# Optimization experiments

Measured on AMD Instinct MI355X. Metric: run time of the kernel, lower is better.

## Reference

```python
import jax, jax.numpy as jnp
import numpy as np

EPS = 1e-5  # torch BatchNorm default eps


def _bn(x, gamma, beta, axes):
    # training-mode batch norm over `axes`, channel dim is axis 1
    mean = jnp.mean(x, axis=axes, keepdims=True)
    var = jnp.var(x, axis=axes, keepdims=True)
    shape = [1] * x.ndim
    shape[1] = -1
    return (x - mean) * jax.lax.rsqrt(var + EPS) * gamma.reshape(shape) + beta.reshape(shape)


def setup_inputs() -> dict:
    B, C, N = 16, 512, 192
    S_RATIO, R_RATIO = 4, 8
    Cs, Cr = C // S_RATIO, C // R_RATIO  # 128, 64
    inter = N * Cr + C  # 12800
    key = jax.random.key(0)
    ks = jax.random.split(key, 6)

    def w(k, shp, fan):
        return jax.random.normal(k, shp, jnp.float32) * np.float32(np.sqrt(2.0 / fan))

    return {
        "inputs": jax.random.normal(ks[0], (B, C, N), jnp.float32),
        "retain": 0,
        "theta_w": w(ks[1], (Cs, C), Cs), "theta_b": jnp.zeros((Cs,), jnp.float32),
        "theta_g": jnp.ones((Cs,), jnp.float32), "theta_be": jnp.zeros((Cs,), jnp.float32),
        "phi_w": w(ks[2], (Cs, C), Cs), "phi_b": jnp.zeros((Cs,), jnp.float32),
        "phi_g": jnp.ones((Cs,), jnp.float32), "phi_be": jnp.zeros((Cs,), jnp.float32),
        "re_w": w(ks[3], (Cr, Cs), Cr), "re_b": jnp.zeros((Cr,), jnp.float32),
        "re_g": jnp.ones((Cr,), jnp.float32), "re_be": jnp.zeros((Cr,), jnp.float32),
        "att_w": w(ks[4], (C, inter), C), "att_b": jnp.zeros((C,), jnp.float32),
        "att_g": jnp.ones((C,), jnp.float32), "att_be": jnp.zeros((C,), jnp.float32),
    }


def reference(inputs, retain, theta_w, theta_b, theta_g, theta_be,
              phi_w, phi_b, phi_g, phi_be, re_w, re_b, re_g, re_be,
              att_w, att_b, att_g, att_be):
    B, C, N = inputs.shape
    xt = inputs.transpose(0, 2, 1)  # [B, N, C]

    # theta / phi pro_blocks: Linear -> BN1d (over B,N) -> ReLU, output [B, Cs, N]
    th = jax.nn.relu(_bn(jnp.einsum('bnc,oc->bon', xt, theta_w) + theta_b[None, :, None], theta_g, theta_be, (0, 2)))
    ph = jax.nn.relu(_bn(jnp.einsum('bnc,oc->bon', xt, phi_w) + phi_b[None, :, None], phi_g, phi_be, (0, 2)))
    th = th.transpose(0, 2, 1)  # [B, N, Cs]
    ph = ph.transpose(0, 2, 1)  # [B, N, Cs]

    # pairwise broadcast-diff: [B, N, N, Cs]
    diff = th[:, :, None, :] - ph[:, None, :, :]

    # pro_block1: Linear -> BN2d -> ReLU, then flatten to [B, N, N*Cr]
    rel = jnp.einsum('bijc,oc->boij', diff, re_w) + re_b[None, :, None, None]  # [B, Cr, N, N]
    rel = jax.nn.relu(_bn(rel, re_g, re_be, (0, 2, 3)))
    rel = rel.transpose(0, 2, 3, 1).reshape(B, N, -1)  # [B, N, N*Cr]

    # attention_generator: Linear -> BN1d -> sigmoid, output [B, C, N]
    cat = jnp.concatenate([xt, rel], axis=2)  # [B, N, C + N*Cr]
    att = jnp.einsum('bni,oi->bon', cat, att_w) + att_b[None, :, None]  # [B, C, N]
    att = jax.nn.sigmoid(_bn(att, att_g, att_be, (0, 2)))

    features = att * inputs  # [B, C, N]
    if retain:
        return features
    return jnp.sum(features, axis=2) / jnp.sum(att, axis=2)  # [B, C]
```

## Files before the change

kernel.cpp:

```cpp
#include <hip/hip_runtime.h>

#define BB 16
#define CC 512
#define NN 192
#define CS 128
#define CR 64
#define EPSF 1e-5f
#define PART (BB*CC*NN)

typedef __attribute__((ext_vector_type(8))) short short8;
typedef __attribute__((ext_vector_type(4))) float f32x4;
typedef __attribute__((ext_vector_type(4))) unsigned int uint4v;

#define OFF_LIN2  0
#define OFF_ATTPX 0
#define OFF_A     1572864
#define OFF_B     1769472
#define OFF_P2    1966080
#define OFF_QT    2162688
#define OFF_ATTP3 2359296
#define OFF_WBF   7077888
#define OFF_XT    10354688
#define OFF_ROWS  11141120
#define OFF_SCL   11157504

__device__ __forceinline__ unsigned pkbf(float a, float b){
  unsigned r; asm("v_cvt_pk_bf16_f32 %0, %1, %2" : "=v"(r) : "v"(a), "v"(b)); return r;
}

__device__ __forceinline__ void gload_lds16(const void* g, void* l){
  __builtin_amdgcn_global_load_lds(
      (const __attribute__((address_space(1))) unsigned int*)g,
      (__attribute__((address_space(3))) unsigned int*)l, 16, 0, 0);
}

__global__ __launch_bounds__(256) void kconvxt(
    const float* __restrict__ aw, const float* __restrict__ x,
    short* __restrict__ wbf, short* __restrict__ xT)
{
  __shared__ float Ts[64][65];
  if (blockIdx.x < 3200) {
    int t = blockIdx.x*256 + threadIdx.x;
    int o2 = t / 1600;
    int kk = (t - o2*1600) * 8;
    const float* src = &aw[o2*12800 + kk];
    float4 v0 = *reinterpret_cast<const float4*>(src);
    float4 v1 = *reinterpret_cast<const float4*>(src+4);
    uint4v w;
    w.x = pkbf(v0.x, v0.y); w.y = pkbf(v0.z, v0.w);
    w.z = pkbf(v1.x, v1.y); w.w = pkbf(v1.z, v1.w);
    *reinterpret_cast<uint4v*>(&wbf[o2*12800 + kk]) = w;
  } else {
    int bid = blockIdx.x - 3200;
    int nt = bid % 3; int ct = (bid/3) & 7; int b = bid / 24;
    int c0 = ct*64, n0 = nt*64;
    int tid = threadIdx.x;
    int col = tid & 63, r0 = tid >> 6;
    #pragma unroll
    for (int it = 0; it < 16; ++it){
      int r = r0 + it*4;
      Ts[r][col] = x[(b*CC + c0 + r)*NN + n0 + col];
    }
    __syncthreads();
    #pragma unroll
    for (int it = 0; it < 2; ++it){
      int cp = it*256 + tid;
      int nr = cp >> 3, cc8 = (cp & 7)*8;
      uint4v wv;
      wv.x = pkbf(Ts[cc8+0][nr], Ts[cc8+1][nr]);
      wv.y = pkbf(Ts[cc8+2][nr], Ts[cc8+3][nr]);
      wv.z = pkbf(Ts[cc8+4][nr], Ts[cc8+5][nr]);
      wv.w = pkbf(Ts[cc8+6][nr], Ts[cc8+7][nr]);
      *reinterpret_cast<uint4v*>(&xT[((b*NN) + n0 + nr)*CC + c0 + cc8]) = wv;
    }
  }
}

__global__ __launch_bounds__(256) void k1_lin(
    const float* __restrict__ x, const float* __restrict__ wth,
    const float* __restrict__ wph, float* __restrict__ lin2)
{
  int bid = blockIdx.x;
  int nt = bid % 3; int ch = (bid/3) & 1; int b = (bid/6) & 15; int path = bid/96;
  int cs0 = ch*64, n0 = nt*64;
  const float* w = path ? wph : wth;
  int tid = threadIdx.x;
  int ty = tid >> 4, tx = tid & 15;
  __shared__ float Xs[32][64];
  __shared__ float Ws[32][68];
  float acc[4][4];
  #pragma unroll
  for (int i=0;i<4;++i)
    #pragma unroll
    for (int j=0;j<4;++j) acc[i][j]=0.f;
  for (int c0 = 0; c0 < CC; c0 += 32){
    __syncthreads();
    {
      int nn = tid & 63, cb = tid >> 6;
      #pragma unroll
      for (int it = 0; it < 8; ++it)
        Xs[cb + it*4][nn] = x[(b*CC + c0 + cb + it*4)*NN + n0 + nn];
    }
    {
      int cc = tid & 31, sb = tid >> 5;
      #pragma unroll
      for (int it = 0; it < 8; ++it)
        Ws[cc][sb + it*8] = w[(cs0 + sb + it*8)*CC + c0 + cc];
    }
    __syncthreads();
    #pragma unroll 8
    for (int cc = 0; cc < 32; ++cc){
      float w4[4], x4[4];
      *reinterpret_cast<float4*>(w4) = *reinterpret_cast<const float4*>(&Ws[cc][ty*4]);
      *reinterpret_cast<float4*>(x4) = *reinterpret_cast<const float4*>(&Xs[cc][tx*4]);
      #pragma unroll
      for (int i=0;i<4;++i)
        #pragma unroll
        for (int j=0;j<4;++j) acc[i][j] += w4[i]*x4[j];
    }
  }
  #pragma unroll
  for (int r = 0; r < 4; ++r){
    int cs = cs0 + ty*4 + r;
    float4 v = make_float4(acc[r][0],acc[r][1],acc[r][2],acc[r][3]);
    *reinterpret_cast<float4*>(&lin2[(b*256 + path*128 + cs)*NN + n0 + tx*4]) = v;
  }
}

__global__ __launch_bounds__(256) void k2_stats(
    const float* __restrict__ lin2,
    const float* __restrict__ tg, const float* __restrict__ tbe,
    const float* __restrict__ pg, const float* __restrict__ pbe,
    float* __restrict__ scl)
{
  int cs2 = blockIdx.x;
  const float* src = lin2 + cs2*NN;
  int tid = threadIdx.x;
  float s=0.f, q=0.f;
  for (int e = tid; e < BB*NN; e += 256){
    int b = e / NN, n = e - b*NN;
    float v = src[b*256*NN + n];
    s += v; q += v*v;
  }
  __shared__ float rs[4], rq[4];
  #pragma unroll
  for (int off=32; off; off>>=1){ s += __shfl_down(s,off); q += __shfl_down(q,off); }
  int w = tid >> 6;
  if ((tid & 63)==0){ rs[w]=s; rq[w]=q; }
  __syncthreads();
  if (tid==0){
    s = rs[0]+rs[1]+rs[2]+rs[3]; q = rq[0]+rq[1]+rq[2]+rq[3];
    float mean = s * (1.f/3072.f);
    float var = q * (1.f/3072.f) - mean*mean;
    int path = cs2 >> 7, c = cs2 & 127;
    float g  = path ? pg[c]  : tg[c];
    float be = path ? pbe[c] : tbe[c];
    float a = g * rsqrtf(var + EPSF);
    scl[cs2] = a; scl[256+cs2] = be - mean*a;
  }
}

__global__ __launch_bounds__(256) void k3_gemm(
    const float* __restrict__ lin2, const float* __restrict__ scl,
    const float* __restrict__ rw,
    float* __restrict__ A, float* __restrict__ Bq, float* __restrict__ rows4)
{
  int bid = blockIdx.x;
  int ih = bid & 3; int b = (bid>>2) & 15; int path = bid >> 6;
  int i0 = ih*48;
  __shared__ float Ls[128][48];
  __shared__ float Ws[64][132];
  int tid = threadIdx.x;
  #pragma unroll
  for (int it = 0; it < 6; ++it){
    int cp = it*256 + tid;
    int row = cp / 12, c4 = cp - row*12;
    float a = scl[path*128 + row], d = scl[256 + path*128 + row];
    float4 v = *reinterpret_cast<const float4*>(&lin2[(b*256 + path*128 + row)*NN + i0 + c4*4]);
    float4 r;
    r.x = fmaxf(a*v.x + d, 0.f); r.y = fmaxf(a*v.y + d, 0.f);
    r.z = fmaxf(a*v.z + d, 0.f); r.w = fmaxf(a*v.w + d, 0.f);
    *reinterpret_cast<float4*>(&Ls[row][c4*4]) = r;
  }
  #pragma unroll
  for (int it = 0; it < 8; ++it){
    int cp = it*256 + tid;
    int o = cp >> 5, c4 = cp & 31;
    *reinterpret_cast<float4*>(&Ws[o][c4*4]) =
      *reinterpret_cast<const float4*>(&rw[o*CS + c4*4]);
  }
  __syncthreads();
  int oy = tid >> 4, ix = tid & 15;
  float acc[4][3];
  #pragma unroll
  for (int r=0;r<4;++r)
    #pragma unroll
    for (int e=0;e<3;++e) acc[r][e]=0.f;
  #pragma unroll 4
  for (int c = 0; c < 128; ++c){
    float w4[4], l3[3];
    #pragma unroll
    for (int r=0;r<4;++r) w4[r] = Ws[oy*4+r][c];
    #pragma unroll
    for (int e=0;e<3;++e) l3[e] = Ls[c][ix*3+e];
    #pragma unroll
    for (int r=0;r<4;++r)
      #pragma unroll
      for (int e=0;e<3;++e) acc[r][e] += w4[r]*l3[e];
  }
  float* dst = path ? Bq : A;
  #pragma unroll
  for (int r=0;r<4;++r)
    #pragma unroll
    for (int e=0;e<3;++e)
      dst[(b*CR + oy*4+r)*NN + i0 + ix*3 + e] = acc[r][e];
  #pragma unroll
  for (int r=0;r<4;++r){
    float s = acc[r][0]+acc[r][1]+acc[r][2];
    float q = acc[r][0]*acc[r][0]+acc[r][1]*acc[r][1]+acc[r][2]*acc[r][2];
    #pragma unroll
    for (int off=8; off; off>>=1){ s += __shfl_down(s,off,16); q += __shfl_down(q,off,16); }
    if (ix==0){
      int o = oy*4+r;
      int ri = (path*1024 + b*64 + o)*4 + ih;
      rows4[ri] = s; rows4[8192 + ri] = q;
    }
  }
}

__global__ void k4_relstats(const float* __restrict__ rows4,
    const float* __restrict__ rg, const float* __restrict__ rbe,
    float* __restrict__ scl)
{
  int o = threadIdx.x;
  float sa=0,saq=0,sb=0,sbq=0,cross=0;
  for (int b=0;b<BB;++b){
    float ra=0, rb=0;
    #pragma unroll
    for (int ih=0; ih<4; ++ih){
      int ia = (b*64+o)*4 + ih, ib = (1024 + b*64+o)*4 + ih;
      ra += rows4[ia]; rb += rows4[ib];
      saq += rows4[8192 + ia]; sbq += rows4[8192 + ib];
    }
    sa += ra; sb += rb; cross += ra*rb;
  }
  float mean = (sa - sb) * (1.f/3072.f);
  float e2 = (saq + sbq) * (1.f/3072.f) - cross * (2.f/589824.f);
  float var = e2 - mean*mean;
  float s = rg[o] * rsqrtf(var + EPSF);
  scl[512+o] = s;
  scl[576+o] = rbe[o] - s*mean;
}

__global__ __launch_bounds__(256) void k4_pq(
    const float* __restrict__ A, const float* __restrict__ Bq,
    const float* __restrict__ scl, float* __restrict__ p2,
    float* __restrict__ qT)
{
  int idx = blockIdx.x*256 + threadIdx.x;
  const int TOT = BB*CR*NN;
  int path = idx / TOT; int e = idx - path*TOT;
  int b = e / (CR*NN); int rem = e - b*(CR*NN);
  if (path == 0) {
    int n = rem >> 6, o = rem & 63;
    p2[e] = scl[512+o]*A[b*CR*NN + o*NN + n] + scl[576+o];
  } else {
    int j = rem >> 6, o = rem & 63;
    qT[e] = scl[512+o]*Bq[b*CR*NN + o*NN + j];
  }
}

__global__ __launch_bounds__(256) void k5_mfma(
    const short* __restrict__ wbf, const short* __restrict__ xT,
    const float* __restrict__ p2, const float* __restrict__ qT,
    float* __restrict__ attpx, float* __restrict__ attp3)
{
  int bid = blockIdx.x;
  int nt = bid & 1, mt = (bid >> 1) & 3, b = (bid >> 3) & 15, ks = bid >> 7;
  int o20 = mt*128, n0 = nt*96;
  int j0 = ks*48;

  int tid = threadIdx.x;
  int w = tid >> 6, lane = tid & 63;
  int wr = w >> 1, wc = w & 1;
  int l15 = lane & 15, l4 = lane >> 4;
  int cq = tid & 7;

  __shared__ __align__(16) short As[128*64];
  __shared__ __align__(16) short Bs[96*64];
  __shared__ __align__(16) float qlds[2][64];

  float pr[3][8];
  #pragma unroll
  for (int it=0; it<3; ++it){
    int n = it*32 + (tid >> 3);
    const float* pp = &p2[((b*NN) + n0 + n)*64 + cq*8];
    float4 u0 = *reinterpret_cast<const float4*>(pp);
    float4 u1 = *reinterpret_cast<const float4*>(pp+4);
    pr[it][0]=u0.x; pr[it][1]=u0.y; pr[it][2]=u0.z; pr[it][3]=u0.w;
    pr[it][4]=u1.x; pr[it][5]=u1.y; pr[it][6]=u1.z; pr[it][7]=u1.w;
  }
  if (tid < 64) qlds[0][tid] = qT[(b*NN + j0)*64 + tid];

  auto stageA = [&](int colbase){
    #pragma unroll
    for (int it=0; it<4; ++it){
      int cp = w*256 + it*64 + lane;
      int row = cp >> 3, c = (cp & 7) ^ (row & 7);
      gload_lds16(&wbf[(o20 + row)*12800 + colbase + c*8],
                  &As[(w*256 + it*64)*8]);
    }
  };
  auto stageBx = [&](int colbase){
    #pragma unroll
    for (int it=0; it<3; ++it){
      int cp = w*192 + it*64 + lane;
      int row = cp >> 3, c = (cp & 7) ^ (row & 7);
      gload_lds16(&xT[((b*NN) + n0 + row)*CC + colbase + c*8],
                  &Bs[(w*192 + it*64)*8]);
    }
  };

  f32x4 acc[4][3];
  #pragma unroll
  for (int mi=0;mi<4;++mi)
    #pragma unroll
    for (int ni=0;ni<3;++ni) acc[mi][ni] = (f32x4){0.f,0.f,0.f,0.f};

  auto mfma_phase = [&](){
    #pragma unroll
    for (int s=0; s<2; ++s){
      short8 av[4], bv[3];
      int c = s*4 + l4;
      #pragma unroll
      for (int mi=0; mi<4; ++mi){
        int row = wr*64 + mi*16 + l15;
        av[mi] = *reinterpret_cast<const short8*>(&As[row*64 + ((c ^ (row&7))<<3)]);
      }
      #pragma unroll
      for (int ni=0; ni<3; ++ni){
        int rown = wc*48 + ni*16 + l15;
        bv[ni] = *reinterpret_cast<const short8*>(&Bs[rown*64 + ((c ^ (rown&7))<<3)]);
      }
      #pragma unroll
      for (int mi=0; mi<4; ++mi)
        #pragma unroll
        for (int ni=0; ni<3; ++ni)
          acc[mi][ni] = __builtin_amdgcn_mfma_f32_16x16x32_bf16(av[mi], bv[ni], acc[mi][ni], 0, 0, 0);
    }
  };

  for (int kt = 0; kt < 2; ++kt){
    __syncthreads();
    stageA(ks*128 + kt*64);
    stageBx(ks*128 + kt*64);
    __syncthreads();
    mfma_phase();
  }
  for (int kt = 0; kt < 48; ++kt){
    int j = j0 + kt;
    __syncthreads();
    stageA(512 + j*64);
    if (tid < 64 && kt < 47) qlds[(kt+1)&1][tid] = qT[(b*NN + j + 1)*64 + tid];
    {
      const float* qq = qlds[kt&1];
      float4 qa = *reinterpret_cast<const float4*>(&qq[cq*8]);
      float4 qb = *reinterpret_cast<const float4*>(&qq[cq*8+4]);
      #pragma unroll
      for (int it=0; it<3; ++it){
        float r0 = fmaxf(pr[it][0]-qa.x, 0.f);
        float r1 = fmaxf(pr[it][1]-qa.y, 0.f);
        float r2 = fmaxf(pr[it][2]-qa.z, 0.f);
        float r3 = fmaxf(pr[it][3]-qa.w, 0.f);
        float r4 = fmaxf(pr[it][4]-qb.x, 0.f);
        float r5 = fmaxf(pr[it][5]-qb.y, 0.f);
        float r6 = fmaxf(pr[it][6]-qb.z, 0.f);
        float r7 = fmaxf(pr[it][7]-qb.w, 0.f);
        uint4v wv;
        wv.x = pkbf(r0,r1); wv.y = pkbf(r2,r3);
        wv.z = pkbf(r4,r5); wv.w = pkbf(r6,r7);
        int n = it*32 + (tid >> 3);
        *reinterpret_cast<uint4v*>(&Bs[n*64 + ((cq ^ (n&7))<<3)]) = wv;
      }
    }
    __syncthreads();
    mfma_phase();
  }

  float* dst = (ks == 0) ? attpx : (attp3 + (size_t)(ks-1)*PART);
  #pragma unroll
  for (int mi=0; mi<4; ++mi){
    #pragma unroll
    for (int r=0; r<4; ++r){
      int o2 = o20 + wr*64 + mi*16 + l4*4 + r;
      #pragma unroll
      for (int ni=0; ni<3; ++ni){
        int n = n0 + wc*48 + ni*16 + l15;
        dst[(b*CC + o2)*NN + n] = acc[mi][ni][r];
      }
    }
  }
}

__global__ __launch_bounds__(256) void k67(
    const float* __restrict__ px, const float* __restrict__ p3,
    const float* __restrict__ x,
    const float* __restrict__ g, const float* __restrict__ be,
    float* __restrict__ out)
{
  int o2 = blockIdx.x;
  int tid = threadIdx.x;
  int b = tid >> 4, nl = tid & 15;
  int base = (b*CC + o2)*NN + nl;
  float v[12], xv[12];
  float s=0.f, q=0.f;
  #pragma unroll
  for (int it=0; it<12; ++it){
    int idx = base + it*16;
    float t = px[idx] + p3[idx] + p3[PART+idx] + p3[2*PART+idx];
    v[it] = t; s += t; q += t*t;
    xv[it] = x[idx];
  }
  __shared__ float rs[4], rq[4], ad[2];
  #pragma unroll
  for (int off=32; off; off>>=1){ s += __shfl_down(s,off); q += __shfl_down(q,off); }
  int w = tid >> 6;
  if ((tid & 63)==0){ rs[w]=s; rq[w]=q; }
  __syncthreads();
  if (tid==0){
    s = rs[0]+rs[1]+rs[2]+rs[3]; q = rq[0]+rq[1]+rq[2]+rq[3];
    float mean = s * (1.f/3072.f);
    float var = q * (1.f/3072.f) - mean*mean;
    float a = g[o2] * rsqrtf(var + EPSF);
    ad[0] = a; ad[1] = be[o2] - mean*a;
  }
  __syncthreads();
  float a = ad[0], d = ad[1];
  float sf=0.f, ss=0.f;
  #pragma unroll
  for (int it=0; it<12; ++it){
    float sig = 1.f/(1.f + expf(-(a*v[it] + d)));
    sf += sig * xv[it]; ss += sig;
  }
  #pragma unroll
  for (int off=8; off; off>>=1){ sf += __shfl_down(sf,off,16); ss += __shfl_down(ss,off,16); }
  if (nl==0) out[b*CC + o2] = sf/ss;
}

extern "C" void kernel_launch(void* const* d_in, const int* in_sizes, int n_in,
                              void* d_out, int out_size, void* d_ws, size_t ws_size,
                              hipStream_t stream)
{
  const float* inputs  = (const float*)d_in[0];
  const float* theta_w = (const float*)d_in[2];
  const float* theta_g = (const float*)d_in[4];
  const float* theta_be= (const float*)d_in[5];
  const float* phi_w   = (const float*)d_in[6];
  const float* phi_g   = (const float*)d_in[8];
  const float* phi_be  = (const float*)d_in[9];
  const float* re_w    = (const float*)d_in[10];
  const float* re_g    = (const float*)d_in[12];
  const float* re_be   = (const float*)d_in[13];
  const float* att_w   = (const float*)d_in[14];
  const float* att_g   = (const float*)d_in[16];
  const float* att_be  = (const float*)d_in[17];

  float* ws = (float*)d_ws;
  float* lin2  = ws + OFF_LIN2;
  float* attpx = ws + OFF_ATTPX;
  float* Abuf  = ws + OFF_A;
  float* Bbuf  = ws + OFF_B;
  float* p2buf = ws + OFF_P2;
  float* qTbuf = ws + OFF_QT;
  float* attp3 = ws + OFF_ATTP3;
  short* wbf   = (short*)(ws + OFF_WBF);
  short* xT    = (short*)(ws + OFF_XT);
  float* rows4 = ws + OFF_ROWS;
  float* scl   = ws + OFF_SCL;

  kconvxt<<<3584, 256, 0, stream>>>(att_w, inputs, wbf, xT);
  k1_lin<<<192, 256, 0, stream>>>(inputs, theta_w, phi_w, lin2);
  k2_stats<<<256, 256, 0, stream>>>(lin2, theta_g, theta_be, phi_g, phi_be, scl);
  k3_gemm<<<128, 256, 0, stream>>>(lin2, scl, re_w, Abuf, Bbuf, rows4);
  k4_relstats<<<1, 64, 0, stream>>>(rows4, re_g, re_be, scl);
  k4_pq<<<1536, 256, 0, stream>>>(Abuf, Bbuf, scl, p2buf, qTbuf);
  k5_mfma<<<512, 256, 0, stream>>>(wbf, xT, p2buf, qTbuf, attpx, attp3);
  k67<<<512, 256, 0, stream>>>(attpx, attp3, inputs, att_g, att_be, (float*)d_out);
}
```

Baseline: 136.0 us.

## Fuse BN stats into linear kernel, drop pq kernel, build B operands in registers

Computes per-channel partial sums inside k1_lin and replaces the stats kernel with a single-block finalize. k3_gemm now writes raw p/q in transposed layout, and the BN scale/shift is applied inside k5_mfma, which removes the separate k4_pq kernel. k5_mfma also builds its B operand fragments directly in registers instead of staging them through LDS, which drops the Bs buffer and its stores and reads. The aim is fewer launches, less global traffic and less LDS traffic. The cost is more register pressure in k5, now with a launch-bounds hint, and uncoalesced short8 global loads of xT.

```diff
diff --git a/kernel.cpp b/kernel.cpp
--- a/kernel.cpp
+++ b/kernel.cpp
@@ -14,15 +14,14 @@
 
 #define OFF_LIN2  0
 #define OFF_ATTPX 0
-#define OFF_A     1572864
-#define OFF_B     1769472
-#define OFF_P2    1966080
-#define OFF_QT    2162688
-#define OFF_ATTP3 2359296
-#define OFF_WBF   7077888
-#define OFF_XT    10354688
-#define OFF_ROWS  11141120
-#define OFF_SCL   11157504
+#define OFF_P2    1572864
+#define OFF_QT    1769472
+#define OFF_ATTP3 1966080
+#define OFF_WBF   6684672
+#define OFF_XT    9961472
+#define OFF_ROWS  10747904
+#define OFF_SPART 10764288
+#define OFF_SCL   10788864
 
 __device__ __forceinline__ unsigned pkbf(float a, float b){
   unsigned r; asm("v_cvt_pk_bf16_f32 %0, %1, %2" : "=v"(r) : "v"(a), "v"(b)); return r;
@@ -78,7 +77,8 @@
 
 __global__ __launch_bounds__(256) void k1_lin(
     const float* __restrict__ x, const float* __restrict__ wth,
-    const float* __restrict__ wph, float* __restrict__ lin2)
+    const float* __restrict__ wph, float* __restrict__ lin2,
+    float* __restrict__ spart)
 {
   int bid = blockIdx.x;
   int nt = bid % 3; int ch = (bid/3) & 1; int b = (bid/6) & 15; int path = bid/96;
@@ -125,45 +125,44 @@
     float4 v = make_float4(acc[r][0],acc[r][1],acc[r][2],acc[r][3]);
     *reinterpret_cast<float4*>(&lin2[(b*256 + path*128 + cs)*NN + n0 + tx*4]) = v;
   }
-}
-
-__global__ __launch_bounds__(256) void k2_stats(
-    const float* __restrict__ lin2,
+  #pragma unroll
+  for (int r = 0; r < 4; ++r){
+    float s = acc[r][0]+acc[r][1]+acc[r][2]+acc[r][3];
+    float q = acc[r][0]*acc[r][0]+acc[r][1]*acc[r][1]
+            + acc[r][2]*acc[r][2]+acc[r][3]*acc[r][3];
+    #pragma unroll
+    for (int off=8; off; off>>=1){ s += __shfl_down(s,off,16); q += __shfl_down(q,off,16); }
+    if (tx==0){
+      int cs2 = path*128 + cs0 + ty*4 + r;
+      spart[cs2*48 + b*3 + nt] = s;
+      spart[12288 + cs2*48 + b*3 + nt] = q;
+    }
+  }
+}
+
+__global__ void k2_fin(const float* __restrict__ spart,
     const float* __restrict__ tg, const float* __restrict__ tbe,
     const float* __restrict__ pg, const float* __restrict__ pbe,
     float* __restrict__ scl)
 {
-  int cs2 = blockIdx.x;
-  const float* src = lin2 + cs2*NN;
-  int tid = threadIdx.x;
+  int c2 = threadIdx.x;
   float s=0.f, q=0.f;
-  for (int e = tid; e < BB*NN; e += 256){
-    int b = e / NN, n = e - b*NN;
-    float v = src[b*256*NN + n];
-    s += v; q += v*v;
-  }
-  __shared__ float rs[4], rq[4];
-  #pragma unroll
-  for (int off=32; off; off>>=1){ s += __shfl_down(s,off); q += __shfl_down(q,off); }
-  int w = tid >> 6;
-  if ((tid & 63)==0){ rs[w]=s; rq[w]=q; }
-  __syncthreads();
-  if (tid==0){
-    s = rs[0]+rs[1]+rs[2]+rs[3]; q = rq[0]+rq[1]+rq[2]+rq[3];
-    float mean = s * (1.f/3072.f);
-    float var = q * (1.f/3072.f) - mean*mean;
-    int path = cs2 >> 7, c = cs2 & 127;
-    float g  = path ? pg[c]  : tg[c];
-    float be = path ? pbe[c] : tbe[c];
-    float a = g * rsqrtf(var + EPSF);
-    scl[cs2] = a; scl[256+cs2] = be - mean*a;
-  }
+  #pragma unroll 8
+  for (int i=0;i<48;++i){ s += spart[c2*48+i]; q += spart[12288+c2*48+i]; }
+  float mean = s * (1.f/3072.f);
+  float var = q * (1.f/3072.f) - mean*mean;
+  int path = c2 >> 7, c = c2 & 127;
+  float g  = path ? pg[c]  : tg[c];
+  float be = path ? pbe[c] : tbe[c];
+  float a = g * rsqrtf(var + EPSF);
+  scl[c2] = a; scl[256+c2] = be - mean*a;
 }
 
 __global__ __launch_bounds__(256) void k3_gemm(
     const float* __restrict__ lin2, const float* __restrict__ scl,
     const float* __restrict__ rw,
-    float* __restrict__ A, float* __restrict__ Bq, float* __restrict__ rows4)
+    float* __restrict__ p2raw, float* __restrict__ qTraw,
+    float* __restrict__ rows4)
 {
   int bid = blockIdx.x;
   int ih = bid & 3; int b = (bid>>2) & 15; int path = bid >> 6;
@@ -208,12 +207,12 @@
       #pragma unroll
       for (int e=0;e<3;++e) acc[r][e] += w4[r]*l3[e];
   }
-  float* dst = path ? Bq : A;
+  float* dst = path ? qTraw : p2raw;
   #pragma unroll
   for (int r=0;r<4;++r)
     #pragma unroll
     for (int e=0;e<3;++e)
-      dst[(b*CR + oy*4+r)*NN + i0 + ix*3 + e] = acc[r][e];
+      dst[(b*NN + i0 + ix*3 + e)*64 + oy*4 + r] = acc[r][e];
   #pragma unroll
   for (int r=0;r<4;++r){
     float s = acc[r][0]+acc[r][1]+acc[r][2];
@@ -252,27 +251,10 @@
   scl[576+o] = rbe[o] - s*mean;
 }
 
-__global__ __launch_bounds__(256) void k4_pq(
-    const float* __restrict__ A, const float* __restrict__ Bq,
-    const float* __restrict__ scl, float* __restrict__ p2,
-    float* __restrict__ qT)
-{
-  int idx = blockIdx.x*256 + threadIdx.x;
-  const int TOT = BB*CR*NN;
-  int path = idx / TOT; int e = idx - path*TOT;
-  int b = e / (CR*NN); int rem = e - b*(CR*NN);
-  if (path == 0) {
-    int n = rem >> 6, o = rem & 63;
-    p2[e] = scl[512+o]*A[b*CR*NN + o*NN + n] + scl[576+o];
-  } else {
-    int j = rem >> 6, o = rem & 63;
-    qT[e] = scl[512+o]*Bq[b*CR*NN + o*NN + j];
-  }
-}
-
-__global__ __launch_bounds__(256) void k5_mfma(
+__global__ __launch_bounds__(256, 2) void k5_mfma(
     const short* __restrict__ wbf, const short* __restrict__ xT,
-    const float* __restrict__ p2, const float* __restrict__ qT,
+    const float* __restrict__ p2raw, const float* __restrict__ qTraw,
+    const float* __restrict__ scl,
     float* __restrict__ attpx, float* __restrict__ attp3)
 {
   int bid = blockIdx.x;
@@ -284,23 +266,36 @@
   int w = tid >> 6, lane = tid & 63;
   int wr = w >> 1, wc = w & 1;
   int l15 = lane & 15, l4 = lane >> 4;
-  int cq = tid & 7;
+  int ob = l4*8;
 
   __shared__ __align__(16) short As[128*64];
-  __shared__ __align__(16) short Bs[96*64];
   __shared__ __align__(16) float qlds[2][64];
 
-  float pr[3][8];
-  #pragma unroll
-  for (int it=0; it<3; ++it){
-    int n = it*32 + (tid >> 3);
-    const float* pp = &p2[((b*NN) + n0 + n)*64 + cq*8];
-    float4 u0 = *reinterpret_cast<const float4*>(pp);
-    float4 u1 = *reinterpret_cast<const float4*>(pp+4);
-    pr[it][0]=u0.x; pr[it][1]=u0.y; pr[it][2]=u0.z; pr[it][3]=u0.w;
-    pr[it][4]=u1.x; pr[it][5]=u1.y; pr[it][6]=u1.z; pr[it][7]=u1.w;
-  }
-  if (tid < 64) qlds[0][tid] = qT[(b*NN + j0)*64 + tid];
+  float sq_ = scl[512 + (tid & 63)];
+
+  float pa[3][16];
+  {
+    float sc[16], sh[16];
+    *reinterpret_cast<float4*>(&sc[0])  = *reinterpret_cast<const float4*>(&scl[512+ob]);
+    *reinterpret_cast<float4*>(&sc[4])  = *reinterpret_cast<const float4*>(&scl[512+ob+4]);
+    *reinterpret_cast<float4*>(&sc[8])  = *reinterpret_cast<const float4*>(&scl[512+32+ob]);
+    *reinterpret_cast<float4*>(&sc[12]) = *reinterpret_cast<const float4*>(&scl[512+32+ob+4]);
+    *reinterpret_cast<float4*>(&sh[0])  = *reinterpret_cast<const float4*>(&scl[576+ob]);
+    *reinterpret_cast<float4*>(&sh[4])  = *reinterpret_cast<const float4*>(&scl[576+ob+4]);
+    *reinterpret_cast<float4*>(&sh[8])  = *reinterpret_cast<const float4*>(&scl[576+32+ob]);
+    *reinterpret_cast<float4*>(&sh[12]) = *reinterpret_cast<const float4*>(&scl[576+32+ob+4]);
+    #pragma unroll
+    for (int ni=0; ni<3; ++ni){
+      const float* pb = &p2raw[(size_t)((b*NN) + n0 + wc*48 + ni*16 + l15)*64];
+      float r[16];
+      *reinterpret_cast<float4*>(&r[0])  = *reinterpret_cast<const float4*>(&pb[ob]);
+      *reinterpret_cast<float4*>(&r[4])  = *reinterpret_cast<const float4*>(&pb[ob+4]);
+      *reinterpret_cast<float4*>(&r[8])  = *reinterpret_cast<const float4*>(&pb[32+ob]);
+      *reinterpret_cast<float4*>(&r[12]) = *reinterpret_cast<const float4*>(&pb[32+ob+4]);
+      #pragma unroll
+      for (int k=0;k<16;++k) pa[ni][k] = sc[k]*r[k] + sh[k];
+    }
+  }
 
   auto stageA = [&](int colbase){
     #pragma unroll
@@ -311,15 +306,6 @@
                   &As[(w*256 + it*64)*8]);
     }
   };
-  auto stageBx = [&](int colbase){
-    #pragma unroll
-    for (int it=0; it<3; ++it){
-      int cp = w*192 + it*64 + lane;
-      int row = cp >> 3, c = (cp & 7) ^ (row & 7);
-      gload_lds16(&xT[((b*NN) + n0 + row)*CC + colbase + c*8],
-                  &Bs[(w*192 + it*64)*8]);
-    }
-  };
 
   f32x4 acc[4][3];
   #pragma unroll
@@ -327,10 +313,10 @@
     #pragma unroll
     for (int ni=0;ni<3;++ni) acc[mi][ni] = (f32x4){0.f,0.f,0.f,0.f};
 
-  auto mfma_phase = [&](){
+  auto mfma_phase = [&](short8 bvv[3][2]){
     #pragma unroll
     for (int s=0; s<2; ++s){
-      short8 av[4], bv[3];
+      short8 av[4];
       int c = s*4 + l4;
       #pragma unroll
       for (int mi=0; mi<4; ++mi){
@@ -338,53 +324,61 @@
         av[mi] = *reinterpret_cast<const short8*>(&As[row*64 + ((c ^ (row&7))<<3)]);
       }
       #pragma unroll
-      for (int ni=0; ni<3; ++ni){
-        int rown = wc*48 + ni*16 + l15;
-        bv[ni] = *reinterpret_cast<const short8*>(&Bs[rown*64 + ((c ^ (rown&7))<<3)]);
-      }
-      #pragma unroll
       for (int mi=0; mi<4; ++mi)
         #pragma unroll
         for (int ni=0; ni<3; ++ni)
-          acc[mi][ni] = __builtin_amdgcn_mfma_f32_16x16x32_bf16(av[mi], bv[ni], acc[mi][ni], 0, 0, 0);
+          acc[mi][ni] = __builtin_amdgcn_mfma_f32_16x16x32_bf16(av[mi], bvv[ni][s], acc[mi][ni], 0, 0, 0);
     }
   };
 
-  for (int kt = 0; kt < 2; ++kt){
+  stageA(ks*128);
+  if (tid < 64) qlds[0][tid] = sq_ * qTraw[(size_t)(b*NN + j0)*64 + tid];
+  short8 bvx[3][2];
+  #pragma unroll
+  for (int ni=0; ni<3; ++ni)
+    #pragma unroll
+    for (int s=0; s<2; ++s)
+      bvx[ni][s] = *reinterpret_cast<const short8*>(
+        &xT[(size_t)((b*NN) + n0 + wc*48 + ni*16 + l15)*CC + ks*128 + s*32 + ob]);
+  __syncthreads();
+  mfma_phase(bvx);
+  __syncthreads();
+  stageA(ks*128 + 64);
+  #pragma unroll
+  for (int ni=0; ni<3; ++ni)
+    #pragma unroll
+    for (int s=0; s<2; ++s)
+      bvx[ni][s] = *reinterpret_cast<const short8*>(
+        &xT[(size_t)((b*NN) + n0 + wc*48 + ni*16 + l15)*CC + ks*128 + 64 + s*32 + ob]);
+  __syncthreads();
+  mfma_phase(bvx);
+
+  for (int kt = 0; kt < 48; ++kt){
     __syncthreads();
-    stageA(ks*128 + kt*64);
-    stageBx(ks*128 + kt*64);
+    stageA(512 + (j0 + kt)*64);
+    if (tid < 64 && kt < 47)
+      qlds[(kt+1)&1][tid] = sq_ * qTraw[(size_t)(b*NN + j0 + kt + 1)*64 + tid];
+    const float* qq = qlds[kt&1];
+    float ql[16];
+    *reinterpret_cast<float4*>(&ql[0])  = *reinterpret_cast<const float4*>(&qq[ob]);
+    *reinterpret_cast<float4*>(&ql[4])  = *reinterpret_cast<const float4*>(&qq[ob+4]);
+    *reinterpret_cast<float4*>(&ql[8])  = *reinterpret_cast<const float4*>(&qq[32+ob]);
+    *reinterpret_cast<float4*>(&ql[12]) = *reinterpret_cast<const float4*>(&qq[32+ob+4]);
+    short8 bvv[3][2];
+    #pragma unroll
+    for (int ni=0; ni<3; ++ni){
+      #pragma unroll
+      for (int s=0; s<2; ++s){
+        uint4v u;
+        u.x = pkbf(fmaxf(pa[ni][s*8+0]-ql[s*8+0],0.f), fmaxf(pa[ni][s*8+1]-ql[s*8+1],0.f));
+        u.y = pkbf(fmaxf(pa[ni][s*8+2]-ql[s*8+2],0.f), fmaxf(pa[ni][s*8+3]-ql[s*8+3],0.f));
+        u.z = pkbf(fmaxf(pa[ni][s*8+4]-ql[s*8+4],0.f), fmaxf(pa[ni][s*8+5]-ql[s*8+5],0.f));
+        u.w = pkbf(fmaxf(pa[ni][s*8+6]-ql[s*8+6],0.f), fmaxf(pa[ni][s*8+7]-ql[s*8+7],0.f));
+        bvv[ni][s] = *reinterpret_cast<short8*>(&u);
+      }
+    }
     __syncthreads();
-    mfma_phase();
-  }
-  for (int kt = 0; kt < 48; ++kt){
-    int j = j0 + kt;
-    __syncthreads();
-    stageA(512 + j*64);
-    if (tid < 64 && kt < 47) qlds[(kt+1)&1][tid] = qT[(b*NN + j + 1)*64 + tid];
-    {
-      const float* qq = qlds[kt&1];
-      float4 qa = *reinterpret_cast<const float4*>(&qq[cq*8]);
-      float4 qb = *reinterpret_cast<const float4*>(&qq[cq*8+4]);
-      #pragma unroll
-      for (int it=0; it<3; ++it){
-        float r0 = fmaxf(pr[it][0]-qa.x, 0.f);
-        float r1 = fmaxf(pr[it][1]-qa.y, 0.f);
-        float r2 = fmaxf(pr[it][2]-qa.z, 0.f);
-        float r3 = fmaxf(pr[it][3]-qa.w, 0.f);
-        float r4 = fmaxf(pr[it][4]-qb.x, 0.f);
-        float r5 = fmaxf(pr[it][5]-qb.y, 0.f);
-        float r6 = fmaxf(pr[it][6]-qb.z, 0.f);
-        float r7 = fmaxf(pr[it][7]-qb.w, 0.f);
-        uint4v wv;
-        wv.x = pkbf(r0,r1); wv.y = pkbf(r2,r3);
-        wv.z = pkbf(r4,r5); wv.w = pkbf(r6,r7);
-        int n = it*32 + (tid >> 3);
-        *reinterpret_cast<uint4v*>(&Bs[n*64 + ((cq ^ (n&7))<<3)]) = wv;
-      }
-    }
-    __syncthreads();
-    mfma_phase();
+    mfma_phase(bvv);
   }
 
   float* dst = (ks == 0) ? attpx : (attp3 + (size_t)(ks-1)*PART);
@@ -468,22 +462,20 @@
   float* ws = (float*)d_ws;
   float* lin2  = ws + OFF_LIN2;
   float* attpx = ws + OFF_ATTPX;
-  float* Abuf  = ws + OFF_A;
-  float* Bbuf  = ws + OFF_B;
-  float* p2buf = ws + OFF_P2;
-  float* qTbuf = ws + OFF_QT;
+  float* p2raw = ws + OFF_P2;
+  float* qTraw = ws + OFF_QT;
   float* attp3 = ws + OFF_ATTP3;
   short* wbf   = (short*)(ws + OFF_WBF);
   short* xT    = (short*)(ws + OFF_XT);
   float* rows4 = ws + OFF_ROWS;
+  float* spart = ws + OFF_SPART;
   float* scl   = ws + OFF_SCL;
 
+  k1_lin<<<192, 256, 0, stream>>>(inputs, theta_w, phi_w, lin2, spart);
   kconvxt<<<3584, 256, 0, stream>>>(att_w, inputs, wbf, xT);
-  k1_lin<<<192, 256, 0, stream>>>(inputs, theta_w, phi_w, lin2);
-  k2_stats<<<256, 256, 0, stream>>>(lin2, theta_g, theta_be, phi_g, phi_be, scl);
-  k3_gemm<<<128, 256, 0, stream>>>(lin2, scl, re_w, Abuf, Bbuf, rows4);
+  k2_fin<<<1, 256, 0, stream>>>(spart, theta_g, theta_be, phi_g, phi_be, scl);
+  k3_gemm<<<128, 256, 0, stream>>>(lin2, scl, re_w, p2raw, qTraw, rows4);
   k4_relstats<<<1, 64, 0, stream>>>(rows4, re_g, re_be, scl);
-  k4_pq<<<1536, 256, 0, stream>>>(Abuf, Bbuf, scl, p2buf, qTbuf);
-  k5_mfma<<<512, 256, 0, stream>>>(wbf, xT, p2buf, qTbuf, attpx, attp3);
+  k5_mfma<<<512, 256, 0, stream>>>(wbf, xT, p2raw, qTraw, scl, attpx, attp3);
   k67<<<512, 256, 0, stream>>>(attpx, attp3, inputs, att_g, att_be, (float*)d_out);
 }
```

Result: slower. 140.6 us (+3.4%).

## Fuse prep/linear/stats kernels, fold BN scaling into GEMM, split K wider with atomics

Applied to the files above, without the earlier changes.

Merges the weight/transpose conversion and theta/phi linear into one launch. That launch emits per-tile partial BN statistics, which the relation GEMM reduces itself, removing the separate stats kernel. The relation BN stats and p/q scaling kernels are folded into the main MFMA kernel, which now uses 8 K-splits and 1024 blocks. Results accumulate via atomicAdd into four zeroed partial buffers, which requires a memset of those buffers. The change cuts launch count and intermediate traffic, at the cost of redundant per-block stat reductions, atomic contention and the extra memset.

```diff
diff --git a/kernel.cpp b/kernel.cpp
--- a/kernel.cpp
+++ b/kernel.cpp
@@ -13,16 +13,13 @@
 typedef __attribute__((ext_vector_type(4))) unsigned int uint4v;
 
 #define OFF_LIN2  0
-#define OFF_ATTPX 0
-#define OFF_A     1572864
-#define OFF_B     1769472
-#define OFF_P2    1966080
-#define OFF_QT    2162688
-#define OFF_ATTP3 2359296
-#define OFF_WBF   7077888
-#define OFF_XT    10354688
-#define OFF_ROWS  11141120
-#define OFF_SCL   11157504
+#define OFF_P2    786432
+#define OFF_QT    983040
+#define OFF_ATTP4 1179648
+#define OFF_WBF   7471104
+#define OFF_XT    10747904
+#define OFF_ROWS  11534336
+#define OFF_SPART 11550720
 
 __device__ __forceinline__ unsigned pkbf(float a, float b){
   unsigned r; asm("v_cvt_pk_bf16_f32 %0, %1, %2" : "=v"(r) : "v"(a), "v"(b)); return r;
@@ -34,13 +31,16 @@
       (__attribute__((address_space(3))) unsigned int*)l, 16, 0, 0);
 }
 
-__global__ __launch_bounds__(256) void kconvxt(
+__global__ __launch_bounds__(256) void kprep(
     const float* __restrict__ aw, const float* __restrict__ x,
-    short* __restrict__ wbf, short* __restrict__ xT)
+    const float* __restrict__ wth, const float* __restrict__ wph,
+    short* __restrict__ wbf, short* __restrict__ xT,
+    float* __restrict__ lin2, float* __restrict__ spart)
 {
-  __shared__ float Ts[64][65];
+  __shared__ __align__(16) float smem[4224];
+  int tid = threadIdx.x;
   if (blockIdx.x < 3200) {
-    int t = blockIdx.x*256 + threadIdx.x;
+    int t = blockIdx.x*256 + tid;
     int o2 = t / 1600;
     int kk = (t - o2*1600) * 8;
     const float* src = &aw[o2*12800 + kk];
@@ -50,11 +50,11 @@
     w.x = pkbf(v0.x, v0.y); w.y = pkbf(v0.z, v0.w);
     w.z = pkbf(v1.x, v1.y); w.w = pkbf(v1.z, v1.w);
     *reinterpret_cast<uint4v*>(&wbf[o2*12800 + kk]) = w;
-  } else {
+  } else if (blockIdx.x < 3584) {
+    float (*Ts)[65] = reinterpret_cast<float(*)[65]>(smem);
     int bid = blockIdx.x - 3200;
     int nt = bid % 3; int ct = (bid/3) & 7; int b = bid / 24;
     int c0 = ct*64, n0 = nt*64;
-    int tid = threadIdx.x;
     int col = tid & 63, r0 = tid >> 6;
     #pragma unroll
     for (int it = 0; it < 16; ++it){
@@ -73,109 +73,101 @@
       wv.w = pkbf(Ts[cc8+6][nr], Ts[cc8+7][nr]);
       *reinterpret_cast<uint4v*>(&xT[((b*NN) + n0 + nr)*CC + c0 + cc8]) = wv;
     }
-  }
-}
-
-__global__ __launch_bounds__(256) void k1_lin(
-    const float* __restrict__ x, const float* __restrict__ wth,
-    const float* __restrict__ wph, float* __restrict__ lin2)
-{
-  int bid = blockIdx.x;
-  int nt = bid % 3; int ch = (bid/3) & 1; int b = (bid/6) & 15; int path = bid/96;
-  int cs0 = ch*64, n0 = nt*64;
-  const float* w = path ? wph : wth;
-  int tid = threadIdx.x;
-  int ty = tid >> 4, tx = tid & 15;
-  __shared__ float Xs[32][64];
-  __shared__ float Ws[32][68];
-  float acc[4][4];
-  #pragma unroll
-  for (int i=0;i<4;++i)
-    #pragma unroll
-    for (int j=0;j<4;++j) acc[i][j]=0.f;
-  for (int c0 = 0; c0 < CC; c0 += 32){
-    __syncthreads();
-    {
-      int nn = tid & 63, cb = tid >> 6;
-      #pragma unroll
-      for (int it = 0; it < 8; ++it)
-        Xs[cb + it*4][nn] = x[(b*CC + c0 + cb + it*4)*NN + n0 + nn];
-    }
-    {
-      int cc = tid & 31, sb = tid >> 5;
-      #pragma unroll
-      for (int it = 0; it < 8; ++it)
-        Ws[cc][sb + it*8] = w[(cs0 + sb + it*8)*CC + c0 + cc];
-    }
-    __syncthreads();
-    #pragma unroll 8
-    for (int cc = 0; cc < 32; ++cc){
-      float w4[4], x4[4];
-      *reinterpret_cast<float4*>(w4) = *reinterpret_cast<const float4*>(&Ws[cc][ty*4]);
-      *reinterpret_cast<float4*>(x4) = *reinterpret_cast<const float4*>(&Xs[cc][tx*4]);
-      #pragma unroll
-      for (int i=0;i<4;++i)
+  } else {
+    float (*Xs)[64] = reinterpret_cast<float(*)[64]>(smem);
+    float (*Ws)[68] = reinterpret_cast<float(*)[68]>(smem + 2048);
+    int bid = blockIdx.x - 3584;
+    int nt = bid % 3; int ch = (bid/3) & 1; int b = (bid/6) & 15; int path = bid/96;
+    int cs0 = ch*64, n0 = nt*64;
+    const float* w = path ? wph : wth;
+    int ty = tid >> 4, tx = tid & 15;
+    float acc[4][4];
+    #pragma unroll
+    for (int i=0;i<4;++i)
+      #pragma unroll
+      for (int j=0;j<4;++j) acc[i][j]=0.f;
+    for (int c0 = 0; c0 < CC; c0 += 32){
+      __syncthreads();
+      {
+        int nn = tid & 63, cb = tid >> 6;
         #pragma unroll
-        for (int j=0;j<4;++j) acc[i][j] += w4[i]*x4[j];
-    }
-  }
-  #pragma unroll
-  for (int r = 0; r < 4; ++r){
-    int cs = cs0 + ty*4 + r;
-    float4 v = make_float4(acc[r][0],acc[r][1],acc[r][2],acc[r][3]);
-    *reinterpret_cast<float4*>(&lin2[(b*256 + path*128 + cs)*NN + n0 + tx*4]) = v;
-  }
-}
-
-__global__ __launch_bounds__(256) void k2_stats(
-    const float* __restrict__ lin2,
+        for (int it = 0; it < 8; ++it)
+          Xs[cb + it*4][nn] = x[(b*CC + c0 + cb + it*4)*NN + n0 + nn];
+      }
+      {
+        int cc = tid & 31, sb = tid >> 5;
+        #pragma unroll
+        for (int it = 0; it < 8; ++it)
+          Ws[cc][sb + it*8] = w[(cs0 + sb + it*8)*CC + c0 + cc];
+      }
+      __syncthreads();
+      #pragma unroll 8
+      for (int cc = 0; cc < 32; ++cc){
+        float w4[4], x4[4];
+        *reinterpret_cast<float4*>(w4) = *reinterpret_cast<const float4*>(&Ws[cc][ty*4]);
+        *reinterpret_cast<float4*>(x4) = *reinterpret_cast<const float4*>(&Xs[cc][tx*4]);
+        #pragma unroll
+        for (int i=0;i<4;++i)
+          #pragma unroll
+          for (int j=0;j<4;++j) acc[i][j] += w4[i]*x4[j];
+      }
+    }
+    #pragma unroll
+    for (int r = 0; r < 4; ++r){
+      int cs = cs0 + ty*4 + r;
+      float4 v = make_float4(acc[r][0],acc[r][1],acc[r][2],acc[r][3]);
+      *reinterpret_cast<float4*>(&lin2[(b*256 + path*128 + cs)*NN + n0 + tx*4]) = v;
+    }
+    #pragma unroll
+    for (int r = 0; r < 4; ++r){
+      float s = acc[r][0]+acc[r][1]+acc[r][2]+acc[r][3];
+      float q = acc[r][0]*acc[r][0]+acc[r][1]*acc[r][1]
+              + acc[r][2]*acc[r][2]+acc[r][3]*acc[r][3];
+      #pragma unroll
+      for (int off=8; off; off>>=1){ s += __shfl_down(s,off,16); q += __shfl_down(q,off,16); }
+      if (tx==0){
+        int cs2 = path*128 + cs0 + ty*4 + r;
+        spart[cs2*48 + b*3 + nt] = s;
+        spart[12288 + cs2*48 + b*3 + nt] = q;
+      }
+    }
+  }
+}
+
+__global__ __launch_bounds__(256) void k3_gemm(
+    const float* __restrict__ lin2, const float* __restrict__ spart,
     const float* __restrict__ tg, const float* __restrict__ tbe,
     const float* __restrict__ pg, const float* __restrict__ pbe,
-    float* __restrict__ scl)
-{
-  int cs2 = blockIdx.x;
-  const float* src = lin2 + cs2*NN;
-  int tid = threadIdx.x;
-  float s=0.f, q=0.f;
-  for (int e = tid; e < BB*NN; e += 256){
-    int b = e / NN, n = e - b*NN;
-    float v = src[b*256*NN + n];
-    s += v; q += v*v;
-  }
-  __shared__ float rs[4], rq[4];
-  #pragma unroll
-  for (int off=32; off; off>>=1){ s += __shfl_down(s,off); q += __shfl_down(q,off); }
-  int w = tid >> 6;
-  if ((tid & 63)==0){ rs[w]=s; rq[w]=q; }
-  __syncthreads();
-  if (tid==0){
-    s = rs[0]+rs[1]+rs[2]+rs[3]; q = rq[0]+rq[1]+rq[2]+rq[3];
-    float mean = s * (1.f/3072.f);
-    float var = q * (1.f/3072.f) - mean*mean;
-    int path = cs2 >> 7, c = cs2 & 127;
-    float g  = path ? pg[c]  : tg[c];
-    float be = path ? pbe[c] : tbe[c];
-    float a = g * rsqrtf(var + EPSF);
-    scl[cs2] = a; scl[256+cs2] = be - mean*a;
-  }
-}
-
-__global__ __launch_bounds__(256) void k3_gemm(
-    const float* __restrict__ lin2, const float* __restrict__ scl,
     const float* __restrict__ rw,
-    float* __restrict__ A, float* __restrict__ Bq, float* __restrict__ rows4)
+    float* __restrict__ p2raw, float* __restrict__ qTraw,
+    float* __restrict__ rows4)
 {
   int bid = blockIdx.x;
   int ih = bid & 3; int b = (bid>>2) & 15; int path = bid >> 6;
   int i0 = ih*48;
   __shared__ float Ls[128][48];
   __shared__ float Ws[64][132];
+  __shared__ float sscl[512];
   int tid = threadIdx.x;
+  {
+    int c2 = tid;
+    float s=0.f, q=0.f;
+    #pragma unroll 8
+    for (int i=0;i<48;++i){ s += spart[c2*48+i]; q += spart[12288+c2*48+i]; }
+    float mean = s * (1.f/3072.f);
+    float var = q * (1.f/3072.f) - mean*mean;
+    int pth = c2 >> 7, c = c2 & 127;
+    float g  = pth ? pg[c]  : tg[c];
+    float be = pth ? pbe[c] : tbe[c];
+    float a = g * rsqrtf(var + EPSF);
+    sscl[c2] = a; sscl[256+c2] = be - mean*a;
+  }
+  __syncthreads();
   #pragma unroll
   for (int it = 0; it < 6; ++it){
     int cp = it*256 + tid;
     int row = cp / 12, c4 = cp - row*12;
-    float a = scl[path*128 + row], d = scl[256 + path*128 + row];
+    float a = sscl[path*128 + row], d = sscl[256 + path*128 + row];
     float4 v = *reinterpret_cast<const float4*>(&lin2[(b*256 + path*128 + row)*NN + i0 + c4*4]);
     float4 r;
     r.x = fmaxf(a*v.x + d, 0.f); r.y = fmaxf(a*v.y + d, 0.f);
@@ -208,12 +200,12 @@
       #pragma unroll
       for (int e=0;e<3;++e) acc[r][e] += w4[r]*l3[e];
   }
-  float* dst = path ? Bq : A;
+  float* dst = path ? qTraw : p2raw;
   #pragma unroll
   for (int r=0;r<4;++r)
     #pragma unroll
     for (int e=0;e<3;++e)
-      dst[(b*CR + oy*4+r)*NN + i0 + ix*3 + e] = acc[r][e];
+      dst[(b*NN + i0 + ix*3 + e)*64 + oy*4 + r] = acc[r][e];
   #pragma unroll
   for (int r=0;r<4;++r){
     float s = acc[r][0]+acc[r][1]+acc[r][2];
@@ -228,57 +220,17 @@
   }
 }
 
-__global__ void k4_relstats(const float* __restrict__ rows4,
+__global__ __launch_bounds__(256, 4) void k5_mfma(
+    const short* __restrict__ wbf, const short* __restrict__ xT,
+    const float* __restrict__ p2raw, const float* __restrict__ qTraw,
+    const float* __restrict__ rows4,
     const float* __restrict__ rg, const float* __restrict__ rbe,
-    float* __restrict__ scl)
-{
-  int o = threadIdx.x;
-  float sa=0,saq=0,sb=0,sbq=0,cross=0;
-  for (int b=0;b<BB;++b){
-    float ra=0, rb=0;
-    #pragma unroll
-    for (int ih=0; ih<4; ++ih){
-      int ia = (b*64+o)*4 + ih, ib = (1024 + b*64+o)*4 + ih;
-      ra += rows4[ia]; rb += rows4[ib];
-      saq += rows4[8192 + ia]; sbq += rows4[8192 + ib];
-    }
-    sa += ra; sb += rb; cross += ra*rb;
-  }
-  float mean = (sa - sb) * (1.f/3072.f);
-  float e2 = (saq + sbq) * (1.f/3072.f) - cross * (2.f/589824.f);
-  float var = e2 - mean*mean;
-  float s = rg[o] * rsqrtf(var + EPSF);
-  scl[512+o] = s;
-  scl[576+o] = rbe[o] - s*mean;
-}
-
-__global__ __launch_bounds__(256) void k4_pq(
-    const float* __restrict__ A, const float* __restrict__ Bq,
-    const float* __restrict__ scl, float* __restrict__ p2,
-    float* __restrict__ qT)
-{
-  int idx = blockIdx.x*256 + threadIdx.x;
-  const int TOT = BB*CR*NN;
-  int path = idx / TOT; int e = idx - path*TOT;
-  int b = e / (CR*NN); int rem = e - b*(CR*NN);
-  if (path == 0) {
-    int n = rem >> 6, o = rem & 63;
-    p2[e] = scl[512+o]*A[b*CR*NN + o*NN + n] + scl[576+o];
-  } else {
-    int j = rem >> 6, o = rem & 63;
-    qT[e] = scl[512+o]*Bq[b*CR*NN + o*NN + j];
-  }
-}
-
-__global__ __launch_bounds__(256) void k5_mfma(
-    const short* __restrict__ wbf, const short* __restrict__ xT,
-    const float* __restrict__ p2, const float* __restrict__ qT,
-    float* __restrict__ attpx, float* __restrict__ attp3)
+    float* __restrict__ attp4)
 {
   int bid = blockIdx.x;
   int nt = bid & 1, mt = (bid >> 1) & 3, b = (bid >> 3) & 15, ks = bid >> 7;
   int o20 = mt*128, n0 = nt*96;
-  int j0 = ks*48;
+  int j0 = ks*24;
 
   int tid = threadIdx.x;
   int w = tid >> 6, lane = tid & 63;
@@ -289,18 +241,47 @@
   __shared__ __align__(16) short As[128*64];
   __shared__ __align__(16) short Bs[96*64];
   __shared__ __align__(16) float qlds[2][64];
+  __shared__ float srel[128];
+
+  if (tid < 64){
+    int o = tid;
+    float sa=0,saq=0,sb=0,sbq=0,cross=0;
+    for (int bb=0;bb<BB;++bb){
+      float ra=0, rb=0;
+      #pragma unroll
+      for (int ih=0; ih<4; ++ih){
+        int ia = (bb*64+o)*4 + ih, ib = (1024 + bb*64+o)*4 + ih;
+        ra += rows4[ia]; rb += rows4[ib];
+        saq += rows4[8192 + ia]; sbq += rows4[8192 + ib];
+      }
+      sa += ra; sb += rb; cross += ra*rb;
+    }
+    float mean = (sa - sb) * (1.f/3072.f);
+    float e2 = (saq + sbq) * (1.f/3072.f) - cross * (2.f/589824.f);
+    float var = e2 - mean*mean;
+    float s = rg[o] * rsqrtf(var + EPSF);
+    srel[o] = s;
+    srel[64+o] = rbe[o] - s*mean;
+  }
+  __syncthreads();
 
   float pr[3][8];
-  #pragma unroll
-  for (int it=0; it<3; ++it){
-    int n = it*32 + (tid >> 3);
-    const float* pp = &p2[((b*NN) + n0 + n)*64 + cq*8];
-    float4 u0 = *reinterpret_cast<const float4*>(pp);
-    float4 u1 = *reinterpret_cast<const float4*>(pp+4);
-    pr[it][0]=u0.x; pr[it][1]=u0.y; pr[it][2]=u0.z; pr[it][3]=u0.w;
-    pr[it][4]=u1.x; pr[it][5]=u1.y; pr[it][6]=u1.z; pr[it][7]=u1.w;
-  }
-  if (tid < 64) qlds[0][tid] = qT[(b*NN + j0)*64 + tid];
+  {
+    float sc8[8], sh8[8];
+    #pragma unroll
+    for (int k=0;k<8;++k){ sc8[k] = srel[cq*8+k]; sh8[k] = srel[64+cq*8+k]; }
+    #pragma unroll
+    for (int it=0; it<3; ++it){
+      int n = it*32 + (tid >> 3);
+      const float* pp = &p2raw[(size_t)((b*NN) + n0 + n)*64 + cq*8];
+      float4 u0 = *reinterpret_cast<const float4*>(pp);
+      float4 u1 = *reinterpret_cast<const float4*>(pp+4);
+      pr[it][0]=sc8[0]*u0.x+sh8[0]; pr[it][1]=sc8[1]*u0.y+sh8[1];
+      pr[it][2]=sc8[2]*u0.z+sh8[2]; pr[it][3]=sc8[3]*u0.w+sh8[3];
+      pr[it][4]=sc8[4]*u1.x+sh8[4]; pr[it][5]=sc8[5]*u1.y+sh8[5];
+      pr[it][6]=sc8[6]*u1.z+sh8[6]; pr[it][7]=sc8[7]*u1.w+sh8[7];
+    }
+  }
 
   auto stageA = [&](int colbase){
     #pragma unroll
@@ -316,7 +297,7 @@
     for (int it=0; it<3; ++it){
       int cp = w*192 + it*64 + lane;
       int row = cp >> 3, c = (cp & 7) ^ (row & 7);
-      gload_lds16(&xT[((b*NN) + n0 + row)*CC + colbase + c*8],
+      gload_lds16(&xT[(size_t)((b*NN) + n0 + row)*CC + colbase + c*8],
                   &Bs[(w*192 + it*64)*8]);
     }
   };
@@ -328,6 +309,7 @@
     for (int ni=0;ni<3;++ni) acc[mi][ni] = (f32x4){0.f,0.f,0.f,0.f};
 
   auto mfma_phase = [&](){
+    __builtin_amdgcn_s_setprio(1);
     #pragma unroll
     for (int s=0; s<2; ++s){
       short8 av[4], bv[3];
@@ -348,20 +330,20 @@
         for (int ni=0; ni<3; ++ni)
           acc[mi][ni] = __builtin_amdgcn_mfma_f32_16x16x32_bf16(av[mi], bv[ni], acc[mi][ni], 0, 0, 0);
     }
+    __builtin_amdgcn_s_setprio(0);
   };
 
-  for (int kt = 0; kt < 2; ++kt){
+  stageA(ks*64);
+  stageBx(ks*64);
+  if (tid < 64) qlds[0][tid] = srel[tid] * qTraw[(size_t)(b*NN + j0)*64 + tid];
+  __syncthreads();
+  mfma_phase();
+
+  for (int kt = 0; kt < 24; ++kt){
     __syncthreads();
-    stageA(ks*128 + kt*64);
-    stageBx(ks*128 + kt*64);
-    __syncthreads();
-    mfma_phase();
-  }
-  for (int kt = 0; kt < 48; ++kt){
-    int j = j0 + kt;
-    __syncthreads();
-    stageA(512 + j*64);
-    if (tid < 64 && kt < 47) qlds[(kt+1)&1][tid] = qT[(b*NN + j + 1)*64 + tid];
+    stageA(512 + (j0 + kt)*64);
+    if (tid < 64 && kt < 23)
+      qlds[(kt+1)&1][tid] = srel[tid] * qTraw[(size_t)(b*NN + j0 + kt + 1)*64 + tid];
     {
       const float* qq = qlds[kt&1];
       float4 qa = *reinterpret_cast<const float4*>(&qq[cq*8]);
@@ -387,7 +369,7 @@
     mfma_phase();
   }
 
-  float* dst = (ks == 0) ? attpx : (attp3 + (size_t)(ks-1)*PART);
+  float* dst = attp4 + (size_t)(ks & 3)*PART;
   #pragma unroll
   for (int mi=0; mi<4; ++mi){
     #pragma unroll
@@ -396,15 +378,14 @@
       #pragma unroll
       for (int ni=0; ni<3; ++ni){
         int n = n0 + wc*48 + ni*16 + l15;
-        dst[(b*CC + o2)*NN + n] = acc[mi][ni][r];
+        atomicAdd(&dst[(b*CC + o2)*NN + n], acc[mi][ni][r]);
       }
     }
   }
 }
 
 __global__ __launch_bounds__(256) void k67(
-    const float* __restrict__ px, const float* __restrict__ p3,
-    const float* __restrict__ x,
+    const float* __restrict__ p4, const float* __restrict__ x,
     const float* __restrict__ g, const float* __restrict__ be,
     float* __restrict__ out)
 {
@@ -417,7 +398,7 @@
   #pragma unroll
   for (int it=0; it<12; ++it){
     int idx = base + it*16;
-    float t = px[idx] + p3[idx] + p3[PART+idx] + p3[2*PART+idx];
+    float t = p4[idx] + p4[PART+idx] + p4[2*PART+idx] + p4[3*PART+idx];
     v[it] = t; s += t; q += t*t;
     xv[it] = x[idx];
   }
@@ -467,23 +448,18 @@
 
   float* ws = (float*)d_ws;
   float* lin2  = ws + OFF_LIN2;
-  float* attpx = ws + OFF_ATTPX;
-  float* Abuf  = ws + OFF_A;
-  float* Bbuf  = ws + OFF_B;
-  float* p2buf = ws + OFF_P2;
-  float* qTbuf = ws + OFF_QT;
-  float* attp3 = ws + OFF_ATTP3;
+  float* p2raw = ws + OFF_P2;
+  float* qTraw = ws + OFF_QT;
+  float* attp4 = ws + OFF_ATTP4;
   short* wbf   = (short*)(ws + OFF_WBF);
   short* xT    = (short*)(ws + OFF_XT);
   float* rows4 = ws + OFF_ROWS;
-  float* scl   = ws + OFF_SCL;
-
-  kconvxt<<<3584, 256, 0, stream>>>(att_w, inputs, wbf, xT);
-  k1_lin<<<192, 256, 0, stream>>>(inputs, theta_w, phi_w, lin2);
-  k2_stats<<<256, 256, 0, stream>>>(lin2, theta_g, theta_be, phi_g, phi_be, scl);
-  k3_gemm<<<128, 256, 0, stream>>>(lin2, scl, re_w, Abuf, Bbuf, rows4);
-  k4_relstats<<<1, 64, 0, stream>>>(rows4, re_g, re_be, scl);
-  k4_pq<<<1536, 256, 0, stream>>>(Abuf, Bbuf, scl, p2buf, qTbuf);
-  k5_mfma<<<512, 256, 0, stream>>>(wbf, xT, p2buf, qTbuf, attpx, attp3);
-  k67<<<512, 256, 0, stream>>>(attpx, attp3, inputs, att_g, att_be, (float*)d_out);
-}
+  float* spart = ws + OFF_SPART;
+
+  hipMemsetAsync(attp4, 0, (size_t)4*PART*sizeof(float), stream);
+  kprep<<<3776, 256, 0, stream>>>(att_w, inputs, theta_w, phi_w, wbf, xT, lin2, spart);
+  k3_gemm<<<128, 256, 0, stream>>>(lin2, spart, theta_g, theta_be, phi_g, phi_be,
+                                   re_w, p2raw, qTraw, rows4);
+  k5_mfma<<<1024, 256, 0, stream>>>(wbf, xT, p2raw, qTraw, rows4, re_g, re_be, attp4);
+  k67<<<512, 256, 0, stream>>>(attp4, inputs, att_g, att_be, (float*)d_out);
+}
```

Result: slower. 179.7 us (+32.1%).
